# Performance work log

Measured on AMD Instinct MI355X. Metric: run time of the kernel, lower is better.

Reference implementation:

```python
import jax, jax.numpy as jnp
import numpy as np

B, S, D, K, R = 2, 2048, 2048, 8, 8
F_HID = D // 4


def setup_inputs() -> dict:
    key = jax.random.key(0)
    ks = jax.random.split(key, 9)
    h_L = jax.random.normal(ks[0], (B, S, D), jnp.float32)
    masked = jax.random.bernoulli(ks[1], 0.5, (B, S))  # True = masked token

    def lin(k, shape, fan_in):
        bound = 1.0 / np.sqrt(fan_in)
        return jax.random.uniform(k, shape, jnp.float32, -bound, bound)

    W_route = lin(ks[2], (D, K), D)
    b_route = lin(ks[3], (K,), D)
    W1 = lin(ks[4], (K, D, F_HID), D)
    b1 = lin(ks[5], (K, F_HID), D)
    W2 = lin(ks[6], (K, F_HID, D), F_HID)
    b2 = lin(ks[7], (K, D), F_HID)
    return {"h_L": h_L, "masked": masked, "W_route": W_route, "b_route": b_route,
            "W1": W1, "b1": b1, "W2": W2, "b2": b2, "range_r": R}


def _windowed_sum(x, r):
    # x: [B, S, ...]; returns sum over window [a-r, a+r] excluding position a itself.
    S_ = x.shape[1]
    zero = jnp.zeros_like(x[:, :1])
    cs = jnp.concatenate([zero, jnp.cumsum(x, axis=1)], axis=1)  # [B, S+1, ...]
    idx = jnp.arange(S_)
    hi = jnp.clip(idx + r, 0, S_ - 1) + 1
    lo = jnp.clip(idx - r, 0, S_)
    return cs[:, hi] - cs[:, lo] - x


def reference(h_L, masked, W_route, b_route, W1, b1, W2, b2, range_r):
    unm = (~masked).astype(h_L.dtype)  # [B,S], 1.0 at unmasked tokens
    # Per-token, per-expert 2-layer GELU MLP: [B,S,K,D]
    hid = jax.nn.gelu(jnp.einsum('bsd,kdf->bskf', h_L, W1) + b1, approximate=False)
    eo = jnp.einsum('bskf,kfd->bskd', hid, W2) + b2
    # Zero out masked tokens, then windowed neighbor mean (exact-erf GELU above).
    contrib = eo * unm[:, :, None, None]
    win = _windowed_sum(contrib, range_r)          # [B,S,K,D]
    cnt = _windowed_sum(unm, range_r)              # [B,S]
    mean = win / jnp.maximum(cnt, 1.0)[:, :, None, None]
    # Routing weights from the masked token's own hidden state.
    w = jax.nn.softmax(h_L @ W_route + b_route, axis=-1)  # [B,S,K]
    mixed = jnp.einsum('bsk,bskd->bsd', w, mean)
    # LayerNorm over d_model, no affine, eps=1e-5 (torch F.layer_norm default).
    mu = jnp.mean(mixed, axis=-1, keepdims=True)
    var = jnp.mean((mixed - mu) ** 2, axis=-1, keepdims=True)
    ln = (mixed - mu) / jnp.sqrt(var + 1e-5)
    valid = masked & (cnt > 0)
    return jnp.where(valid[:, :, None], ln, jnp.zeros((), h_L.dtype))
```

## Files before the change

### kernel.cpp

```cpp
#include <hip/hip_runtime.h>
#include <math.h>

#define B_ 2
#define S_ 2048
#define T_ (B_*S_)
#define D_ 2048
#define K_ 8
#define F_ 512
#define R_ 8
#define WSEG 16

typedef unsigned short ushort_t;
typedef __attribute__((__ext_vector_type__(8))) __bf16 bf16x8;
typedef __attribute__((__ext_vector_type__(4))) float f32x4;

__device__ __forceinline__ float bf2f(ushort_t u) {
    return __uint_as_float(((unsigned int)u) << 16);
}
__device__ __forceinline__ ushort_t f2bf(float f) {
    unsigned int u = __float_as_uint(f);
    unsigned int r = u + 0x7FFFu + ((u >> 16) & 1u);
    return (ushort_t)(r >> 16);
}
__device__ __forceinline__ float loadF(const void* p, size_t idx, int f32m) {
    if (f32m) return ((const float*)p)[idx];
    return bf2f(((const ushort_t*)p)[idx]);
}

#if defined(__has_builtin)
#if __has_builtin(__builtin_amdgcn_global_load_lds)
#define ASYNC_LDS 1
#endif
#endif
__device__ __forceinline__ void ld16_lds(void* l, const void* g) {
#ifdef ASYNC_LDS
    __builtin_amdgcn_global_load_lds((const __attribute__((address_space(1))) unsigned int*)g,
                                     (__attribute__((address_space(3))) unsigned int*)l,
                                     16, 0, 0);
#else
    *(uint4*)l = *(const uint4*)g;
#endif
}

__global__ void detect_kernel(const unsigned char* __restrict__ hraw,
                              const unsigned char* __restrict__ mraw,
                              int* __restrict__ modePtr) {
    __shared__ int has_non01, has_nz123, has_3F1, outlier;
    if (threadIdx.x == 0) { has_non01 = 0; has_nz123 = 0; has_3F1 = 0; outlier = 0; }
    __syncthreads();
    int a = 0, b = 0, c = 0, o = 0;
    for (int i = threadIdx.x; i < 4096; i += 256) {
        unsigned char v = mraw[i];
        if (v > 1) a = 1;
        if ((i & 3) != 0 && v != 0) b = 1;
        if ((i & 3) == 1 && v >= 2) c = 1;
        if ((i & 3) == 1) {
            unsigned char hb = hraw[i] & 0x7F;
            if (hb < 0x30 || hb > 0x47) o++;
        }
    }
    if (a) atomicOr(&has_non01, 1);
    if (b) atomicOr(&has_nz123, 1);
    if (c) atomicOr(&has_3F1, 1);
    if (o) atomicAdd(&outlier, o);
    __syncthreads();
    if (threadIdx.x == 0) {
        int mode;
        if (!has_non01) mode = has_nz123 ? 0 : 1;
        else            mode = has_3F1 ? 2 : 3;
        modePtr[0] = mode;
        modePtr[1] = (outlier > 256) ? 1 : 0;
    }
}

__global__ __launch_bounds__(256) void mask_prep_kernel(const void* __restrict__ raw,
                                                        const int* __restrict__ modePtr,
                                                        int* __restrict__ maskI,
                                                        int* __restrict__ idx,
                                                        int* __restrict__ TcPtr,
                                                        float* __restrict__ invcnt,
                                                        int* __restrict__ valid) {
    __shared__ int sm[T_];
    __shared__ int cnts[257];
    const int tid = threadIdx.x;
    const int mode = modePtr[0];
    for (int t = tid; t < T_; t += 256) {
        int m;
        if (mode == 0)      m = ((const unsigned char*)raw)[t] != 0;
        else if (mode == 1) m = ((const int*)raw)[t] != 0;
        else if (mode == 2) m = ((const ushort_t*)raw)[t] != 0;
        else                m = ((const unsigned int*)raw)[t] != 0;
        sm[t] = m;
        maskI[t] = m;
    }
    __syncthreads();
    const int base = tid * 16;
    int cnt = 0;
#pragma unroll
    for (int u = 0; u < 16; ++u) cnt += (sm[base + u] == 0);
    cnts[tid] = cnt;
    __syncthreads();
    if (tid == 0) {
        int run = 0;
        for (int i = 0; i < 256; ++i) { int c = cnts[i]; cnts[i] = run; run += c; }
        cnts[256] = run;
    }
    __syncthreads();
    int run = cnts[tid];
#pragma unroll
    for (int u = 0; u < 16; ++u) {
        int t = base + u;
        if (!sm[t]) idx[run++] = t;
    }
    const int Tc = cnts[256];
    for (int i = Tc + tid; i < T_; i += 256) idx[i] = T_;
    if (tid == 0) TcPtr[0] = Tc;
    for (int t = tid; t < T_; t += 256) {
        int b = t >> 11, s = t & (S_ - 1);
        int lo = s - R_; if (lo < 0) lo = 0;
        int hi = s + R_; if (hi > S_ - 1) hi = S_ - 1;
        int c = 0;
        for (int sp = lo; sp <= hi; ++sp) c += (sm[b * S_ + sp] == 0);
        c -= (sm[t] == 0);
        invcnt[t] = 1.0f / fmaxf((float)c, 1.0f);
        valid[t] = (sm[t] && c > 0) ? 1 : 0;
    }
}

__global__ __launch_bounds__(256) void conv_hc_kernel(const void* __restrict__ hraw,
                                                      const int* __restrict__ modePtr,
                                                      const int* __restrict__ idx,
                                                      const int* __restrict__ TcPtr,
                                                      ushort_t* __restrict__ hbfc) {
    int gid = blockIdx.x * 256 + threadIdx.x;
    int i = gid >> 8;
    if (i >= *TcPtr) return;
    int col = (gid & 255) * 8;
    size_t src = (size_t)idx[i] * D_ + col;
    size_t dst = (size_t)i * D_ + col;
    if (modePtr[1]) {
        const float* p = (const float*)hraw + src;
        float4 a = *(const float4*)p;
        float4 b = *(const float4*)(p + 4);
        uint4 o;
        o.x = (unsigned)f2bf(a.x) | ((unsigned)f2bf(a.y) << 16);
        o.y = (unsigned)f2bf(a.z) | ((unsigned)f2bf(a.w) << 16);
        o.z = (unsigned)f2bf(b.x) | ((unsigned)f2bf(b.y) << 16);
        o.w = (unsigned)f2bf(b.z) | ((unsigned)f2bf(b.w) << 16);
        *(uint4*)&hbfc[dst] = o;
    } else {
        *(uint4*)&hbfc[dst] = *(const uint4*)((const ushort_t*)hraw + src);
    }
}

__global__ __launch_bounds__(256) void router_kernel(const void* __restrict__ hraw,
                                                     const void* __restrict__ Wr,
                                                     const void* __restrict__ br,
                                                     const int* __restrict__ modePtr,
                                                     const int* __restrict__ maskI,
                                                     float* __restrict__ wout) {
    int t = blockIdx.x;
    if (!maskI[t]) return;
    int f32m = modePtr[1];
    float p[8];
#pragma unroll
    for (int k = 0; k < 8; ++k) p[k] = 0.f;
    if (f32m) {
        for (int d = threadIdx.x; d < D_; d += 256) {
            float hv = ((const float*)hraw)[(size_t)t * D_ + d];
            const float* wrow = (const float*)Wr + (size_t)d * 8;
            float4 q0 = *(const float4*)wrow;
            float4 q1 = *(const float4*)(wrow + 4);
            p[0] += hv * q0.x; p[1] += hv * q0.y; p[2] += hv * q0.z; p[3] += hv * q0.w;
            p[4] += hv * q1.x; p[5] += hv * q1.y; p[6] += hv * q1.z; p[7] += hv * q1.w;
        }
    } else {
        const ushort_t* Wrb = (const ushort_t*)Wr;
        for (int d = threadIdx.x; d < D_; d += 256) {
            float hv = bf2f(((const ushort_t*)hraw)[(size_t)t * D_ + d]);
            uint4 q = *(const uint4*)&Wrb[(size_t)d * 8];
            p[0] += hv * __uint_as_float(q.x << 16);
            p[1] += hv * __uint_as_float(q.x & 0xFFFF0000u);
            p[2] += hv * __uint_as_float(q.y << 16);
            p[3] += hv * __uint_as_float(q.y & 0xFFFF0000u);
            p[4] += hv * __uint_as_float(q.z << 16);
            p[5] += hv * __uint_as_float(q.z & 0xFFFF0000u);
            p[6] += hv * __uint_as_float(q.w << 16);
            p[7] += hv * __uint_as_float(q.w & 0xFFFF0000u);
        }
    }
#pragma unroll
    for (int off = 32; off; off >>= 1)
#pragma unroll
        for (int k = 0; k < 8; ++k) p[k] += __shfl_down(p[k], off);
    __shared__ float sm[4][8];
    int w = threadIdx.x >> 6, lane = threadIdx.x & 63;
    if (lane == 0)
#pragma unroll
        for (int k = 0; k < 8; ++k) sm[w][k] = p[k];
    __syncthreads();
    if (threadIdx.x == 0) {
        float lg[8];
        float mx = -1e30f;
#pragma unroll
        for (int k = 0; k < 8; ++k) {
            lg[k] = sm[0][k] + sm[1][k] + sm[2][k] + sm[3][k] + loadF(br, k, f32m);
            mx = fmaxf(mx, lg[k]);
        }
        float ssum = 0.f;
#pragma unroll
        for (int k = 0; k < 8; ++k) { lg[k] = __expf(lg[k] - mx); ssum += lg[k]; }
        float inv = 1.0f / ssum;
#pragma unroll
        for (int k = 0; k < 8; ++k) wout[t * 8 + k] = lg[k] * inv;
    }
}

__global__ __launch_bounds__(256) void transpose_kernel(const void* __restrict__ in,
                                                        ushort_t* __restrict__ op,
                                                        int rows, int cols,
                                                        const int* __restrict__ modePtr) {
    __shared__ ushort_t tile[32][33];
    int f32m = modePtr[1];
    int kexp = blockIdx.z;
    size_t base = (size_t)kexp * rows * cols;
    ushort_t* ob = op + (size_t)kexp * rows * cols;
    int r0 = blockIdx.x * 32, c0 = blockIdx.y * 32;
    int tx = threadIdx.x & 31, ty = threadIdx.x >> 5;
#pragma unroll
    for (int i = 0; i < 4; ++i) {
        int r = ty + i * 8;
        tile[r][tx] = f2bf(loadF(in, base + (size_t)(r0 + r) * cols + c0 + tx, f32m));
    }
    __syncthreads();
#pragma unroll
    for (int i = 0; i < 4; ++i) {
        int c = ty + i * 8;
        ob[(size_t)(c0 + c) * rows + r0 + tx] = tile[tx][c];
    }
}

__global__ __launch_bounds__(256) void gemm1_kernel(const ushort_t* __restrict__ hbfc,
                                                    const ushort_t* __restrict__ W1t,
                                                    const void* __restrict__ b1,
                                                    const int* __restrict__ modePtr,
                                                    const int* __restrict__ TcPtr,
                                                    ushort_t* __restrict__ hidc) {
    const int bm = blockIdx.x;
    if (bm * 128 >= *TcPtr) return;
    __shared__ ushort_t Al[128 * 32];
    __shared__ ushort_t Bl[128 * 32];
    const int f32m = modePtr[1];
    const int kexp = blockIdx.z;
    const int bn = blockIdx.y;
    const int tid = threadIdx.x;
    const int lane = tid & 63, w = tid >> 6;
    const int lm = lane & 15, quad = lane >> 4;
    const int wm = (w >> 1) * 64, wn = (w & 1) * 64;
    const ushort_t* Ab = hbfc + (size_t)(bm * 128) * D_;
    const ushort_t* Bb = W1t + (size_t)kexp * F_ * D_ + (size_t)(bn * 128) * D_;
    f32x4 acc[4][4];
    const f32x4 zz = {0.f, 0.f, 0.f, 0.f};
#pragma unroll
    for (int i = 0; i < 4; ++i)
#pragma unroll
        for (int j = 0; j < 4; ++j) acc[i][j] = zz;
    const int r0 = tid >> 2, c0 = (tid & 3) * 8;
    for (int kt = 0; kt < D_ / 32; ++kt) {
        const int kb = kt * 32;
        __syncthreads();
        ld16_lds(&Al[r0 * 32 + c0],        &Ab[(size_t)r0 * D_ + kb + c0]);
        ld16_lds(&Al[(r0 + 64) * 32 + c0], &Ab[(size_t)(r0 + 64) * D_ + kb + c0]);
        ld16_lds(&Bl[r0 * 32 + c0],        &Bb[(size_t)r0 * D_ + kb + c0]);
        ld16_lds(&Bl[(r0 + 64) * 32 + c0], &Bb[(size_t)(r0 + 64) * D_ + kb + c0]);
        __syncthreads();
        bf16x8 af[4], bfr[4];
#pragma unroll
        for (int i = 0; i < 4; ++i) af[i] = *(const bf16x8*)&Al[(wm + i * 16 + lm) * 32 + quad * 8];
#pragma unroll
        for (int j = 0; j < 4; ++j) bfr[j] = *(const bf16x8*)&Bl[(wn + j * 16 + lm) * 32 + quad * 8];
#pragma unroll
        for (int i = 0; i < 4; ++i)
#pragma unroll
            for (int j = 0; j < 4; ++j)
                acc[i][j] = __builtin_amdgcn_mfma_f32_16x16x32_bf16(af[i], bfr[j], acc[i][j], 0, 0, 0);
    }
#pragma unroll
    for (int j = 0; j < 4; ++j) {
        int fg = bn * 128 + wn + j * 16 + lm;
        float bias = loadF(b1, (size_t)kexp * F_ + fg, f32m);
#pragma unroll
        for (int i = 0; i < 4; ++i) {
            int mb = bm * 128 + wm + i * 16 + quad * 4;
#pragma unroll
            for (int v = 0; v < 4; ++v) {
                float x = acc[i][j][v] + bias;
                float g = 0.5f * x * (1.0f + erff(x * 0.70710678118654752f));
                hidc[(size_t)kexp * T_ * F_ + (size_t)(mb + v) * F_ + fg] = f2bf(g);
            }
        }
    }
}

__global__ __launch_bounds__(256) void gemm2_kernel(const ushort_t* __restrict__ hidc,
                                                    const ushort_t* __restrict__ W2t,
                                                    const void* __restrict__ b2,
                                                    const int* __restrict__ modePtr,
                                                    const int* __restrict__ TcPtr,
                                                    const int* __restrict__ idx,
                                                    ushort_t* __restrict__ eo) {
    const int bm = blockIdx.x;
    if (bm * 128 >= *TcPtr) return;
    __shared__ ushort_t Al[128 * 32];
    __shared__ ushort_t Bl[128 * 32];
    __shared__ int sidx[128];
    const int f32m = modePtr[1];
    const int kexp = blockIdx.z;
    const int bn = blockIdx.y;
    const int tid = threadIdx.x;
    if (tid < 128) sidx[tid] = idx[bm * 128 + tid];
    const int lane = tid & 63, w = tid >> 6;
    const int lm = lane & 15, quad = lane >> 4;
    const int wm = (w >> 1) * 64, wn = (w & 1) * 64;
    const ushort_t* Ab = hidc + (size_t)kexp * T_ * F_ + (size_t)(bm * 128) * F_;
    const ushort_t* Bb = W2t + (size_t)kexp * D_ * F_ + (size_t)(bn * 128) * F_;
    f32x4 acc[4][4];
    const f32x4 zz = {0.f, 0.f, 0.f, 0.f};
#pragma unroll
    for (int i = 0; i < 4; ++i)
#pragma unroll
        for (int j = 0; j < 4; ++j) acc[i][j] = zz;
    const int r0 = tid >> 2, c0 = (tid & 3) * 8;
    for (int kt = 0; kt < F_ / 32; ++kt) {
        const int kb = kt * 32;
        __syncthreads();
        ld16_lds(&Al[r0 * 32 + c0],        &Ab[(size_t)r0 * F_ + kb + c0]);
        ld16_lds(&Al[(r0 + 64) * 32 + c0], &Ab[(size_t)(r0 + 64) * F_ + kb + c0]);
        ld16_lds(&Bl[r0 * 32 + c0],        &Bb[(size_t)r0 * F_ + kb + c0]);
        ld16_lds(&Bl[(r0 + 64) * 32 + c0], &Bb[(size_t)(r0 + 64) * F_ + kb + c0]);
        __syncthreads();
        bf16x8 af[4], bfr[4];
#pragma unroll
        for (int i = 0; i < 4; ++i) af[i] = *(const bf16x8*)&Al[(wm + i * 16 + lm) * 32 + quad * 8];
#pragma unroll
        for (int j = 0; j < 4; ++j) bfr[j] = *(const bf16x8*)&Bl[(wn + j * 16 + lm) * 32 + quad * 8];
#pragma unroll
        for (int i = 0; i < 4; ++i)
#pragma unroll
            for (int j = 0; j < 4; ++j)
                acc[i][j] = __builtin_amdgcn_mfma_f32_16x16x32_bf16(af[i], bfr[j], acc[i][j], 0, 0, 0);
    }
#pragma unroll
    for (int j = 0; j < 4; ++j) {
        int dg = bn * 128 + wn + j * 16 + lm;
        float bias = loadF(b2, (size_t)kexp * D_ + dg, f32m);
#pragma unroll
        for (int i = 0; i < 4; ++i) {
            int lr = wm + i * 16 + quad * 4;
#pragma unroll
            for (int v = 0; v < 4; ++v) {
                int tok = sidx[lr + v];
                float x = acc[i][j][v] + bias;
                eo[((size_t)tok * K_ + kexp) * D_ + dg] = f2bf(x);
            }
        }
    }
}

__device__ __forceinline__ void acc8add(float* run, const ushort_t* p) {
    const uint4 q = *(const uint4*)p;
    run[0] += __uint_as_float(q.x << 16);
    run[1] += __uint_as_float(q.x & 0xFFFF0000u);
    run[2] += __uint_as_float(q.y << 16);
    run[3] += __uint_as_float(q.y & 0xFFFF0000u);
    run[4] += __uint_as_float(q.z << 16);
    run[5] += __uint_as_float(q.z & 0xFFFF0000u);
    run[6] += __uint_as_float(q.w << 16);
    run[7] += __uint_as_float(q.w & 0xFFFF0000u);
}
__device__ __forceinline__ void acc8sub(float* run, const ushort_t* p) {
    const uint4 q = *(const uint4*)p;
    run[0] -= __uint_as_float(q.x << 16);
    run[1] -= __uint_as_float(q.x & 0xFFFF0000u);
    run[2] -= __uint_as_float(q.y << 16);
    run[3] -= __uint_as_float(q.y & 0xFFFF0000u);
    run[4] -= __uint_as_float(q.z << 16);
    run[5] -= __uint_as_float(q.z & 0xFFFF0000u);
    run[6] -= __uint_as_float(q.w << 16);
    run[7] -= __uint_as_float(q.w & 0xFFFF0000u);
}

__global__ __launch_bounds__(256) void window_all_kernel(const ushort_t* __restrict__ eo,
                                                         const float* __restrict__ wR,
                                                         const int* __restrict__ maskI,
                                                         const float* __restrict__ invcnt,
                                                         float* __restrict__ mixed) {
    const int b = blockIdx.y;
    const int s0 = blockIdx.x * WSEG;
    const int d0 = threadIdx.x * 8;
    float run[K_][8];
#pragma unroll
    for (int k = 0; k < K_; ++k)
#pragma unroll
        for (int j = 0; j < 8; ++j) run[k][j] = 0.f;
    int lo = s0 - R_; if (lo < 0) lo = 0;
    for (int sp = lo; sp < s0 + R_; ++sp) {
        if (maskI[b * S_ + sp]) continue;
        const ushort_t* row = &eo[(size_t)(b * S_ + sp) * K_ * D_ + d0];
#pragma unroll
        for (int k = 0; k < K_; ++k) acc8add(run[k], row + (size_t)k * D_);
    }
    for (int s = s0; s < s0 + WSEG; ++s) {
        const int t = b * S_ + s;
        if (s + R_ < S_ && !maskI[t + R_]) {
            const ushort_t* row = &eo[(size_t)(t + R_) * K_ * D_ + d0];
#pragma unroll
            for (int k = 0; k < K_; ++k) acc8add(run[k], row + (size_t)k * D_);
        }
        if (maskI[t]) {
            float ic = invcnt[t];
            float o[8];
#pragma unroll
            for (int j = 0; j < 8; ++j) o[j] = 0.f;
#pragma unroll
            for (int k = 0; k < K_; ++k) {
                float wk = wR[t * K_ + k] * ic;
#pragma unroll
                for (int j = 0; j < 8; ++j) o[j] += wk * run[k][j];
            }
            float4 o0 = {o[0], o[1], o[2], o[3]};
            float4 o1 = {o[4], o[5], o[6], o[7]};
            *(float4*)&mixed[(size_t)t * D_ + d0]     = o0;
            *(float4*)&mixed[(size_t)t * D_ + d0 + 4] = o1;
        }
        if (s - R_ >= 0 && !maskI[t - R_]) {
            const ushort_t* row = &eo[(size_t)(t - R_) * K_ * D_ + d0];
#pragma unroll
            for (int k = 0; k < K_; ++k) acc8sub(run[k], row + (size_t)k * D_);
        }
    }
}

__global__ __launch_bounds__(256) void ln_kernel(const float* __restrict__ mixed,
                                                 const int* __restrict__ valid,
                                                 const int* __restrict__ modePtr,
                                                 void* __restrict__ out) {
    const int t = blockIdx.x;
    const int tid = threadIdx.x;
    const int f32m = modePtr[1];
    if (!valid[t]) {
        if (f32m) {
            float4 z = {0.f, 0.f, 0.f, 0.f};
            float* op = (float*)out + (size_t)t * D_ + tid * 8;
            *(float4*)op = z; *(float4*)(op + 4) = z;
        } else {
            uint4 z = {0u, 0u, 0u, 0u};
            *(uint4*)((ushort_t*)out + (size_t)t * D_ + tid * 8) = z;
        }
        return;
    }
    float4 a = *(const float4*)&mixed[(size_t)t * D_ + tid * 8];
    float4 c = *(const float4*)&mixed[(size_t)t * D_ + tid * 8 + 4];
    float xs[8] = {a.x, a.y, a.z, a.w, c.x, c.y, c.z, c.w};
    float s1 = 0.f, s2 = 0.f;
#pragma unroll
    for (int j = 0; j < 8; ++j) { s1 += xs[j]; s2 += xs[j] * xs[j]; }
#pragma unroll
    for (int off = 32; off; off >>= 1) { s1 += __shfl_down(s1, off); s2 += __shfl_down(s2, off); }
    __shared__ float sm[8];
    int w = tid >> 6;
    if ((tid & 63) == 0) { sm[w * 2] = s1; sm[w * 2 + 1] = s2; }
    __syncthreads();
    float ts1 = sm[0] + sm[2] + sm[4] + sm[6];
    float ts2 = sm[1] + sm[3] + sm[5] + sm[7];
    float mu = ts1 * (1.0f / D_);
    float var = fmaxf(ts2 * (1.0f / D_) - mu * mu, 0.0f);
    float inv = rsqrtf(var + 1e-5f);
    if (f32m) {
        float* op = (float*)out + (size_t)t * D_ + tid * 8;
        float4 o0 = {(xs[0] - mu) * inv, (xs[1] - mu) * inv, (xs[2] - mu) * inv, (xs[3] - mu) * inv};
        float4 o1 = {(xs[4] - mu) * inv, (xs[5] - mu) * inv, (xs[6] - mu) * inv, (xs[7] - mu) * inv};
        *(float4*)op = o0; *(float4*)(op + 4) = o1;
    } else {
        ushort_t ob[8];
#pragma unroll
        for (int j = 0; j < 8; ++j) ob[j] = f2bf((xs[j] - mu) * inv);
        uint4 o;
        o.x = (unsigned)ob[0] | ((unsigned)ob[1] << 16);
        o.y = (unsigned)ob[2] | ((unsigned)ob[3] << 16);
        o.z = (unsigned)ob[4] | ((unsigned)ob[5] << 16);
        o.w = (unsigned)ob[6] | ((unsigned)ob[7] << 16);
        *(uint4*)((ushort_t*)out + (size_t)t * D_ + tid * 8) = o;
    }
}

extern "C" void kernel_launch(void* const* d_in, const int* in_sizes, int n_in,
                              void* d_out, int out_size, void* d_ws, size_t ws_size,
                              hipStream_t stream) {
    const void* h    = d_in[0];
    const void* mraw = d_in[1];
    const void* Wr   = d_in[2];
    const void* br   = d_in[3];
    const void* W1   = d_in[4];
    const void* b1   = d_in[5];
    const void* W2   = d_in[6];
    const void* b2   = d_in[7];
    (void)in_sizes; (void)n_in; (void)out_size; (void)ws_size;

    char* ws = (char*)d_ws;
    size_t off = 0;
    auto alloc = [&](size_t bytes) -> void* {
        void* p = ws + off;
        off += (bytes + 255) & ~(size_t)255;
        return p;
    };
    ushort_t* hbfc  = (ushort_t*)alloc((size_t)T_ * D_ * 2);
    ushort_t* W1t   = (ushort_t*)alloc((size_t)K_ * F_ * D_ * 2);
    ushort_t* W2t   = (ushort_t*)alloc((size_t)K_ * D_ * F_ * 2);
    ushort_t* hidc  = (ushort_t*)alloc((size_t)K_ * T_ * F_ * 2);
    ushort_t* eo    = (ushort_t*)alloc(((size_t)T_ + 1) * K_ * D_ * 2);
    float*    wRbuf = (float*)alloc((size_t)T_ * K_ * 4);
    int*      maskI = (int*)alloc((size_t)T_ * 4);
    float*    invc  = (float*)alloc((size_t)T_ * 4);
    int*      valid = (int*)alloc((size_t)T_ * 4);
    int*      idx   = (int*)alloc((size_t)T_ * 4);
    int*      Tc    = (int*)alloc(256);
    int*      mode  = (int*)alloc(256);
    float*    mixed = (float*)hidc;

    hipLaunchKernelGGL(detect_kernel, dim3(1), dim3(256), 0, stream,
                       (const unsigned char*)h, (const unsigned char*)mraw, mode);
    hipLaunchKernelGGL(mask_prep_kernel, dim3(1), dim3(256), 0, stream,
                       mraw, mode, maskI, idx, Tc, invc, valid);
    hipLaunchKernelGGL(conv_hc_kernel, dim3(T_ * D_ / 8 / 256), dim3(256), 0, stream,
                       h, mode, idx, Tc, hbfc);
    hipLaunchKernelGGL(router_kernel, dim3(T_), dim3(256), 0, stream,
                       h, Wr, br, mode, maskI, wRbuf);
    hipLaunchKernelGGL(transpose_kernel, dim3(D_ / 32, F_ / 32, K_), dim3(256), 0, stream,
                       W1, W1t, D_, F_, mode);
    hipLaunchKernelGGL(transpose_kernel, dim3(F_ / 32, D_ / 32, K_), dim3(256), 0, stream,
                       W2, W2t, F_, D_, mode);
    hipLaunchKernelGGL(gemm1_kernel, dim3(T_ / 128, F_ / 128, K_), dim3(256), 0, stream,
                       hbfc, W1t, b1, mode, Tc, hidc);
    hipLaunchKernelGGL(gemm2_kernel, dim3(T_ / 128, D_ / 128, K_), dim3(256), 0, stream,
                       hidc, W2t, b2, mode, Tc, idx, eo);
    hipLaunchKernelGGL(window_all_kernel, dim3(S_ / WSEG, B_), dim3(256), 0, stream,
                       eo, wRbuf, maskI, invc, mixed);
    hipLaunchKernelGGL(ln_kernel, dim3(T_), dim3(256), 0, stream,
                       mixed, valid, mode, d_out);
}
```

Before: 447.9 us.

## Double-buffer LDS tiles in both expert GEMMs and flatten gemm1 expert grid

Both GEMM kernels now use two LDS buffers, issuing the next K-tile's global-to-LDS loads before the MFMAs on the current tile, with one barrier per iteration instead of two. gemm1 also treats all experts' W1 as a single N=K*F dimension on a 2D grid, taking the expert and feature index from the column. The goal is to hide global load latency behind matrix math and simplify indexing. LDS use per block doubles, which may lower occupancy, and correctness depends on how ld16_lds completes relative to the barrier.

```diff
diff --git a/kernel.cpp b/kernel.cpp
--- a/kernel.cpp
+++ b/kernel.cpp
@@ -248,17 +248,16 @@
                                                     ushort_t* __restrict__ hidc) {
     const int bm = blockIdx.x;
     if (bm * 128 >= *TcPtr) return;
-    __shared__ ushort_t Al[128 * 32];
-    __shared__ ushort_t Bl[128 * 32];
+    __shared__ ushort_t Al[2][128 * 32];
+    __shared__ ushort_t Bl[2][128 * 32];
     const int f32m = modePtr[1];
-    const int kexp = blockIdx.z;
     const int bn = blockIdx.y;
     const int tid = threadIdx.x;
     const int lane = tid & 63, w = tid >> 6;
     const int lm = lane & 15, quad = lane >> 4;
     const int wm = (w >> 1) * 64, wn = (w & 1) * 64;
     const ushort_t* Ab = hbfc + (size_t)(bm * 128) * D_;
-    const ushort_t* Bb = W1t + (size_t)kexp * F_ * D_ + (size_t)(bn * 128) * D_;
+    const ushort_t* Bb = W1t + (size_t)(bn * 128) * D_;
     f32x4 acc[4][4];
     const f32x4 zz = {0.f, 0.f, 0.f, 0.f};
 #pragma unroll
@@ -266,29 +265,39 @@
 #pragma unroll
         for (int j = 0; j < 4; ++j) acc[i][j] = zz;
     const int r0 = tid >> 2, c0 = (tid & 3) * 8;
+    ld16_lds(&Al[0][r0 * 32 + c0],        &Ab[(size_t)r0 * D_ + c0]);
+    ld16_lds(&Al[0][(r0 + 64) * 32 + c0], &Ab[(size_t)(r0 + 64) * D_ + c0]);
+    ld16_lds(&Bl[0][r0 * 32 + c0],        &Bb[(size_t)r0 * D_ + c0]);
+    ld16_lds(&Bl[0][(r0 + 64) * 32 + c0], &Bb[(size_t)(r0 + 64) * D_ + c0]);
+    __syncthreads();
+    int p = 0;
     for (int kt = 0; kt < D_ / 32; ++kt) {
-        const int kb = kt * 32;
-        __syncthreads();
-        ld16_lds(&Al[r0 * 32 + c0],        &Ab[(size_t)r0 * D_ + kb + c0]);
-        ld16_lds(&Al[(r0 + 64) * 32 + c0], &Ab[(size_t)(r0 + 64) * D_ + kb + c0]);
-        ld16_lds(&Bl[r0 * 32 + c0],        &Bb[(size_t)r0 * D_ + kb + c0]);
-        ld16_lds(&Bl[(r0 + 64) * 32 + c0], &Bb[(size_t)(r0 + 64) * D_ + kb + c0]);
-        __syncthreads();
+        const int q = p ^ 1;
+        if (kt + 1 < D_ / 32) {
+            const int kb = (kt + 1) * 32;
+            ld16_lds(&Al[q][r0 * 32 + c0],        &Ab[(size_t)r0 * D_ + kb + c0]);
+            ld16_lds(&Al[q][(r0 + 64) * 32 + c0], &Ab[(size_t)(r0 + 64) * D_ + kb + c0]);
+            ld16_lds(&Bl[q][r0 * 32 + c0],        &Bb[(size_t)r0 * D_ + kb + c0]);
+            ld16_lds(&Bl[q][(r0 + 64) * 32 + c0], &Bb[(size_t)(r0 + 64) * D_ + kb + c0]);
+        }
         bf16x8 af[4], bfr[4];
 #pragma unroll
-        for (int i = 0; i < 4; ++i) af[i] = *(const bf16x8*)&Al[(wm + i * 16 + lm) * 32 + quad * 8];
-#pragma unroll
-        for (int j = 0; j < 4; ++j) bfr[j] = *(const bf16x8*)&Bl[(wn + j * 16 + lm) * 32 + quad * 8];
+        for (int i = 0; i < 4; ++i) af[i] = *(const bf16x8*)&Al[p][(wm + i * 16 + lm) * 32 + quad * 8];
+#pragma unroll
+        for (int j = 0; j < 4; ++j) bfr[j] = *(const bf16x8*)&Bl[p][(wn + j * 16 + lm) * 32 + quad * 8];
 #pragma unroll
         for (int i = 0; i < 4; ++i)
 #pragma unroll
             for (int j = 0; j < 4; ++j)
                 acc[i][j] = __builtin_amdgcn_mfma_f32_16x16x32_bf16(af[i], bfr[j], acc[i][j], 0, 0, 0);
+        __syncthreads();
+        p = q;
     }
 #pragma unroll
     for (int j = 0; j < 4; ++j) {
-        int fg = bn * 128 + wn + j * 16 + lm;
-        float bias = loadF(b1, (size_t)kexp * F_ + fg, f32m);
+        int n = bn * 128 + wn + j * 16 + lm;
+        int kexp = n >> 9, fg = n & 511;
+        float bias = loadF(b1, (size_t)n, f32m);
 #pragma unroll
         for (int i = 0; i < 4; ++i) {
             int mb = bm * 128 + wm + i * 16 + quad * 4;
@@ -311,8 +320,8 @@
                                                     ushort_t* __restrict__ eo) {
     const int bm = blockIdx.x;
     if (bm * 128 >= *TcPtr) return;
-    __shared__ ushort_t Al[128 * 32];
-    __shared__ ushort_t Bl[128 * 32];
+    __shared__ ushort_t Al[2][128 * 32];
+    __shared__ ushort_t Bl[2][128 * 32];
     __shared__ int sidx[128];
     const int f32m = modePtr[1];
     const int kexp = blockIdx.z;
@@ -331,24 +340,33 @@
 #pragma unroll
         for (int j = 0; j < 4; ++j) acc[i][j] = zz;
     const int r0 = tid >> 2, c0 = (tid & 3) * 8;
+    ld16_lds(&Al[0][r0 * 32 + c0],        &Ab[(size_t)r0 * F_ + c0]);
+    ld16_lds(&Al[0][(r0 + 64) * 32 + c0], &Ab[(size_t)(r0 + 64) * F_ + c0]);
+    ld16_lds(&Bl[0][r0 * 32 + c0],        &Bb[(size_t)r0 * F_ + c0]);
+    ld16_lds(&Bl[0][(r0 + 64) * 32 + c0], &Bb[(size_t)(r0 + 64) * F_ + c0]);
+    __syncthreads();
+    int p = 0;
     for (int kt = 0; kt < F_ / 32; ++kt) {
-        const int kb = kt * 32;
-        __syncthreads();
-        ld16_lds(&Al[r0 * 32 + c0],        &Ab[(size_t)r0 * F_ + kb + c0]);
-        ld16_lds(&Al[(r0 + 64) * 32 + c0], &Ab[(size_t)(r0 + 64) * F_ + kb + c0]);
-        ld16_lds(&Bl[r0 * 32 + c0],        &Bb[(size_t)r0 * F_ + kb + c0]);
-        ld16_lds(&Bl[(r0 + 64) * 32 + c0], &Bb[(size_t)(r0 + 64) * F_ + kb + c0]);
-        __syncthreads();
+        const int q = p ^ 1;
+        if (kt + 1 < F_ / 32) {
+            const int kb = (kt + 1) * 32;
+            ld16_lds(&Al[q][r0 * 32 + c0],        &Ab[(size_t)r0 * F_ + kb + c0]);
+            ld16_lds(&Al[q][(r0 + 64) * 32 + c0], &Ab[(size_t)(r0 + 64) * F_ + kb + c0]);
+            ld16_lds(&Bl[q][r0 * 32 + c0],        &Bb[(size_t)r0 * F_ + kb + c0]);
+            ld16_lds(&Bl[q][(r0 + 64) * 32 + c0], &Bb[(size_t)(r0 + 64) * F_ + kb + c0]);
+        }
         bf16x8 af[4], bfr[4];
 #pragma unroll
-        for (int i = 0; i < 4; ++i) af[i] = *(const bf16x8*)&Al[(wm + i * 16 + lm) * 32 + quad * 8];
-#pragma unroll
-        for (int j = 0; j < 4; ++j) bfr[j] = *(const bf16x8*)&Bl[(wn + j * 16 + lm) * 32 + quad * 8];
+        for (int i = 0; i < 4; ++i) af[i] = *(const bf16x8*)&Al[p][(wm + i * 16 + lm) * 32 + quad * 8];
+#pragma unroll
+        for (int j = 0; j < 4; ++j) bfr[j] = *(const bf16x8*)&Bl[p][(wn + j * 16 + lm) * 32 + quad * 8];
 #pragma unroll
         for (int i = 0; i < 4; ++i)
 #pragma unroll
             for (int j = 0; j < 4; ++j)
                 acc[i][j] = __builtin_amdgcn_mfma_f32_16x16x32_bf16(af[i], bfr[j], acc[i][j], 0, 0, 0);
+        __syncthreads();
+        p = q;
     }
 #pragma unroll
     for (int j = 0; j < 4; ++j) {
@@ -540,7 +558,7 @@
                        W1, W1t, D_, F_, mode);
     hipLaunchKernelGGL(transpose_kernel, dim3(F_ / 32, D_ / 32, K_), dim3(256), 0, stream,
                        W2, W2t, F_, D_, mode);
-    hipLaunchKernelGGL(gemm1_kernel, dim3(T_ / 128, F_ / 128, K_), dim3(256), 0, stream,
+    hipLaunchKernelGGL(gemm1_kernel, dim3(T_ / 128, K_ * F_ / 128), dim3(256), 0, stream,
                        hbfc, W1t, b1, mode, Tc, hidc);
     hipLaunchKernelGGL(gemm2_kernel, dim3(T_ / 128, D_ / 128, K_), dim3(256), 0, stream,
                        hidc, W2t, b2, mode, Tc, idx, eo);
```

New measurement: 464.2 us. +3.6%, slower.

## Retile expert GEMMs to 64x128 tiles with K=64 steps and flatten expert dim

Applied to the files above, without the earlier changes.

Both expert GEMMs drop from 128x128 output tiles to 64x128 tiles and stage 64-wide K slices in LDS, so each barrier pair covers two MFMA sub-steps instead of one. The first GEMM now treats all experts as one wide N dimension (K*F columns), deriving expert and hidden index in the epilogue, with grid dimensions adjusted to match. The goals are more blocks for better occupancy and tail behaviour on the compacted token count, and fewer synchronisations per unit of K. The cost is less operand reuse per block, since each loaded B tile now serves only 64 rows, and more LDS per block.

```diff
diff --git a/kernel.cpp b/kernel.cpp
--- a/kernel.cpp
+++ b/kernel.cpp
@@ -247,51 +247,58 @@
                                                     const int* __restrict__ TcPtr,
                                                     ushort_t* __restrict__ hidc) {
     const int bm = blockIdx.x;
-    if (bm * 128 >= *TcPtr) return;
-    __shared__ ushort_t Al[128 * 32];
-    __shared__ ushort_t Bl[128 * 32];
+    if (bm * 64 >= *TcPtr) return;
+    __shared__ ushort_t Al[64 * 64];
+    __shared__ ushort_t Bl[128 * 64];
     const int f32m = modePtr[1];
-    const int kexp = blockIdx.z;
     const int bn = blockIdx.y;
     const int tid = threadIdx.x;
     const int lane = tid & 63, w = tid >> 6;
     const int lm = lane & 15, quad = lane >> 4;
-    const int wm = (w >> 1) * 64, wn = (w & 1) * 64;
-    const ushort_t* Ab = hbfc + (size_t)(bm * 128) * D_;
-    const ushort_t* Bb = W1t + (size_t)kexp * F_ * D_ + (size_t)(bn * 128) * D_;
-    f32x4 acc[4][4];
+    const int wm = (w >> 1) * 32, wn = (w & 1) * 64;
+    const ushort_t* Ab = hbfc + (size_t)(bm * 64) * D_;
+    const ushort_t* Bb = W1t + (size_t)(bn * 128) * D_;
+    f32x4 acc[2][4];
     const f32x4 zz = {0.f, 0.f, 0.f, 0.f};
 #pragma unroll
-    for (int i = 0; i < 4; ++i)
+    for (int i = 0; i < 2; ++i)
 #pragma unroll
         for (int j = 0; j < 4; ++j) acc[i][j] = zz;
-    const int r0 = tid >> 2, c0 = (tid & 3) * 8;
-    for (int kt = 0; kt < D_ / 32; ++kt) {
-        const int kb = kt * 32;
+    const int r0 = tid >> 3, c0 = (tid & 7) * 8;
+    for (int kt = 0; kt < D_ / 64; ++kt) {
+        const int kb = kt * 64;
         __syncthreads();
-        ld16_lds(&Al[r0 * 32 + c0],        &Ab[(size_t)r0 * D_ + kb + c0]);
-        ld16_lds(&Al[(r0 + 64) * 32 + c0], &Ab[(size_t)(r0 + 64) * D_ + kb + c0]);
-        ld16_lds(&Bl[r0 * 32 + c0],        &Bb[(size_t)r0 * D_ + kb + c0]);
-        ld16_lds(&Bl[(r0 + 64) * 32 + c0], &Bb[(size_t)(r0 + 64) * D_ + kb + c0]);
+        ld16_lds(&Al[r0 * 64 + c0],        &Ab[(size_t)r0 * D_ + kb + c0]);
+        ld16_lds(&Al[(r0 + 32) * 64 + c0], &Ab[(size_t)(r0 + 32) * D_ + kb + c0]);
+        ld16_lds(&Bl[r0 * 64 + c0],        &Bb[(size_t)r0 * D_ + kb + c0]);
+        ld16_lds(&Bl[(r0 + 32) * 64 + c0], &Bb[(size_t)(r0 + 32) * D_ + kb + c0]);
+        ld16_lds(&Bl[(r0 + 64) * 64 + c0], &Bb[(size_t)(r0 + 64) * D_ + kb + c0]);
+        ld16_lds(&Bl[(r0 + 96) * 64 + c0], &Bb[(size_t)(r0 + 96) * D_ + kb + c0]);
         __syncthreads();
-        bf16x8 af[4], bfr[4];
-#pragma unroll
-        for (int i = 0; i < 4; ++i) af[i] = *(const bf16x8*)&Al[(wm + i * 16 + lm) * 32 + quad * 8];
-#pragma unroll
-        for (int j = 0; j < 4; ++j) bfr[j] = *(const bf16x8*)&Bl[(wn + j * 16 + lm) * 32 + quad * 8];
-#pragma unroll
-        for (int i = 0; i < 4; ++i)
+#pragma unroll
+        for (int kk = 0; kk < 2; ++kk) {
+            bf16x8 af[2], bfr[4];
+#pragma unroll
+            for (int i = 0; i < 2; ++i)
+                af[i] = *(const bf16x8*)&Al[(wm + i * 16 + lm) * 64 + kk * 32 + quad * 8];
 #pragma unroll
             for (int j = 0; j < 4; ++j)
-                acc[i][j] = __builtin_amdgcn_mfma_f32_16x16x32_bf16(af[i], bfr[j], acc[i][j], 0, 0, 0);
+                bfr[j] = *(const bf16x8*)&Bl[(wn + j * 16 + lm) * 64 + kk * 32 + quad * 8];
+#pragma unroll
+            for (int i = 0; i < 2; ++i)
+#pragma unroll
+                for (int j = 0; j < 4; ++j)
+                    acc[i][j] = __builtin_amdgcn_mfma_f32_16x16x32_bf16(af[i], bfr[j], acc[i][j], 0, 0, 0);
+        }
     }
 #pragma unroll
     for (int j = 0; j < 4; ++j) {
-        int fg = bn * 128 + wn + j * 16 + lm;
-        float bias = loadF(b1, (size_t)kexp * F_ + fg, f32m);
-#pragma unroll
-        for (int i = 0; i < 4; ++i) {
-            int mb = bm * 128 + wm + i * 16 + quad * 4;
+        int n = bn * 128 + wn + j * 16 + lm;
+        int kexp = n >> 9, fg = n & 511;
+        float bias = loadF(b1, (size_t)n, f32m);
+#pragma unroll
+        for (int i = 0; i < 2; ++i) {
+            int mb = bm * 64 + wm + i * 16 + quad * 4;
 #pragma unroll
             for (int v = 0; v < 4; ++v) {
                 float x = acc[i][j][v] + bias;
@@ -310,52 +317,59 @@
                                                     const int* __restrict__ idx,
                                                     ushort_t* __restrict__ eo) {
     const int bm = blockIdx.x;
-    if (bm * 128 >= *TcPtr) return;
-    __shared__ ushort_t Al[128 * 32];
-    __shared__ ushort_t Bl[128 * 32];
-    __shared__ int sidx[128];
+    if (bm * 64 >= *TcPtr) return;
+    __shared__ ushort_t Al[64 * 64];
+    __shared__ ushort_t Bl[128 * 64];
+    __shared__ int sidx[64];
     const int f32m = modePtr[1];
     const int kexp = blockIdx.z;
     const int bn = blockIdx.y;
     const int tid = threadIdx.x;
-    if (tid < 128) sidx[tid] = idx[bm * 128 + tid];
+    if (tid < 64) sidx[tid] = idx[bm * 64 + tid];
     const int lane = tid & 63, w = tid >> 6;
     const int lm = lane & 15, quad = lane >> 4;
-    const int wm = (w >> 1) * 64, wn = (w & 1) * 64;
-    const ushort_t* Ab = hidc + (size_t)kexp * T_ * F_ + (size_t)(bm * 128) * F_;
+    const int wm = (w >> 1) * 32, wn = (w & 1) * 64;
+    const ushort_t* Ab = hidc + (size_t)kexp * T_ * F_ + (size_t)(bm * 64) * F_;
     const ushort_t* Bb = W2t + (size_t)kexp * D_ * F_ + (size_t)(bn * 128) * F_;
-    f32x4 acc[4][4];
+    f32x4 acc[2][4];
     const f32x4 zz = {0.f, 0.f, 0.f, 0.f};
 #pragma unroll
-    for (int i = 0; i < 4; ++i)
+    for (int i = 0; i < 2; ++i)
 #pragma unroll
         for (int j = 0; j < 4; ++j) acc[i][j] = zz;
-    const int r0 = tid >> 2, c0 = (tid & 3) * 8;
-    for (int kt = 0; kt < F_ / 32; ++kt) {
-        const int kb = kt * 32;
+    const int r0 = tid >> 3, c0 = (tid & 7) * 8;
+    for (int kt = 0; kt < F_ / 64; ++kt) {
+        const int kb = kt * 64;
         __syncthreads();
-        ld16_lds(&Al[r0 * 32 + c0],        &Ab[(size_t)r0 * F_ + kb + c0]);
-        ld16_lds(&Al[(r0 + 64) * 32 + c0], &Ab[(size_t)(r0 + 64) * F_ + kb + c0]);
-        ld16_lds(&Bl[r0 * 32 + c0],        &Bb[(size_t)r0 * F_ + kb + c0]);
-        ld16_lds(&Bl[(r0 + 64) * 32 + c0], &Bb[(size_t)(r0 + 64) * F_ + kb + c0]);
+        ld16_lds(&Al[r0 * 64 + c0],        &Ab[(size_t)r0 * F_ + kb + c0]);
+        ld16_lds(&Al[(r0 + 32) * 64 + c0], &Ab[(size_t)(r0 + 32) * F_ + kb + c0]);
+        ld16_lds(&Bl[r0 * 64 + c0],        &Bb[(size_t)r0 * F_ + kb + c0]);
+        ld16_lds(&Bl[(r0 + 32) * 64 + c0], &Bb[(size_t)(r0 + 32) * F_ + kb + c0]);
+        ld16_lds(&Bl[(r0 + 64) * 64 + c0], &Bb[(size_t)(r0 + 64) * F_ + kb + c0]);
+        ld16_lds(&Bl[(r0 + 96) * 64 + c0], &Bb[(size_t)(r0 + 96) * F_ + kb + c0]);
         __syncthreads();
-        bf16x8 af[4], bfr[4];
-#pragma unroll
-        for (int i = 0; i < 4; ++i) af[i] = *(const bf16x8*)&Al[(wm + i * 16 + lm) * 32 + quad * 8];
-#pragma unroll
-        for (int j = 0; j < 4; ++j) bfr[j] = *(const bf16x8*)&Bl[(wn + j * 16 + lm) * 32 + quad * 8];
-#pragma unroll
-        for (int i = 0; i < 4; ++i)
+#pragma unroll
+        for (int kk = 0; kk < 2; ++kk) {
+            bf16x8 af[2], bfr[4];
+#pragma unroll
+            for (int i = 0; i < 2; ++i)
+                af[i] = *(const bf16x8*)&Al[(wm + i * 16 + lm) * 64 + kk * 32 + quad * 8];
 #pragma unroll
             for (int j = 0; j < 4; ++j)
-                acc[i][j] = __builtin_amdgcn_mfma_f32_16x16x32_bf16(af[i], bfr[j], acc[i][j], 0, 0, 0);
+                bfr[j] = *(const bf16x8*)&Bl[(wn + j * 16 + lm) * 64 + kk * 32 + quad * 8];
+#pragma unroll
+            for (int i = 0; i < 2; ++i)
+#pragma unroll
+                for (int j = 0; j < 4; ++j)
+                    acc[i][j] = __builtin_amdgcn_mfma_f32_16x16x32_bf16(af[i], bfr[j], acc[i][j], 0, 0, 0);
+        }
     }
 #pragma unroll
     for (int j = 0; j < 4; ++j) {
         int dg = bn * 128 + wn + j * 16 + lm;
         float bias = loadF(b2, (size_t)kexp * D_ + dg, f32m);
 #pragma unroll
-        for (int i = 0; i < 4; ++i) {
+        for (int i = 0; i < 2; ++i) {
             int lr = wm + i * 16 + quad * 4;
 #pragma unroll
             for (int v = 0; v < 4; ++v) {
@@ -540,9 +554,9 @@
                        W1, W1t, D_, F_, mode);
     hipLaunchKernelGGL(transpose_kernel, dim3(F_ / 32, D_ / 32, K_), dim3(256), 0, stream,
                        W2, W2t, F_, D_, mode);
-    hipLaunchKernelGGL(gemm1_kernel, dim3(T_ / 128, F_ / 128, K_), dim3(256), 0, stream,
+    hipLaunchKernelGGL(gemm1_kernel, dim3(T_ / 64, K_ * F_ / 128), dim3(256), 0, stream,
                        hbfc, W1t, b1, mode, Tc, hidc);
-    hipLaunchKernelGGL(gemm2_kernel, dim3(T_ / 128, D_ / 128, K_), dim3(256), 0, stream,
+    hipLaunchKernelGGL(gemm2_kernel, dim3(T_ / 64, D_ / 128, K_), dim3(256), 0, stream,
                        hidc, W2t, b2, mode, Tc, idx, eo);
     hipLaunchKernelGGL(window_all_kernel, dim3(S_ / WSEG, B_), dim3(256), 0, stream,
                        eo, wRbuf, maskI, invc, mixed);
```

New measurement: 447.2 us. No clear change (-0.2%).
